# Kernel tuning notes

Measured on AMD Instinct MI355X. Metric: run time of the kernel, lower is better.

## Reference

```python
import jax, jax.numpy as jnp
import numpy as np

B, S, H = 4, 256, 768
F = 32            # num_features
T = 256           # TAG_HIDDEN_SIZE
WD = 64           # WIDTH_HIDDEN_SIZE
C = 16            # num_tags


def setup_inputs() -> dict:
    key = jax.random.key(0)
    ks = jax.random.split(key, 10)
    inp = {
        "final_hidden": jax.random.normal(ks[0], (B, S, H), jnp.float32),
        "feature_vecs": jax.random.normal(ks[1], (B, S, F), jnp.float32),
        # Linear params stored [in, out] (transposed vs torch; same math)
        "start_W": jax.random.normal(ks[2], (H + F, T), jnp.float32) * (1.0 / np.sqrt(H + F)),
        "start_b": jnp.zeros((T,), jnp.float32),
        "end_W": jax.random.normal(ks[3], (H + F, T), jnp.float32) * (1.0 / np.sqrt(H + F)),
        "end_b": jnp.zeros((T,), jnp.float32),
        "U": jax.random.normal(ks[4], (T, C, T), jnp.float32) * (1.0 / np.sqrt(T)),
        "width_hidden": jax.random.uniform(ks[5], (S, S, WD), jnp.float32),
        "lin_W": jax.random.normal(ks[6], (2 * T + WD, C), jnp.float32) * (1.0 / np.sqrt(2 * T + WD)),
        "lin_b": jnp.zeros((C,), jnp.float32),
    }
    return inp


def reference(final_hidden, feature_vecs, start_W, start_b, end_W, end_b, U, width_hidden, lin_W, lin_b):
    # dropout p=0.0 -> identity
    x = jnp.concatenate([final_hidden, feature_vecs], axis=-1)   # [B,S,H+F]
    s = x @ start_W + start_b                                    # [B,S,T]
    e = x @ end_W + end_b                                        # [B,S,T]

    # biaffine term: einsum('bsh,hci->bsci') then ('bsci,bei->bsec')
    sU = jnp.einsum('bst,tcu->bscu', s, U)                       # [B,S,C,T]
    pre = jnp.einsum('bscu,beu->bsec', sU, e)                    # [B,S,S,C]

    # pairwise FFN, fused: Linear over concat(start, end, width) decomposes
    # into three small matmuls + broadcast adds (same math, no O(S^2*(2T+W)) buffer)
    Ws, We, Ww = lin_W[:T], lin_W[T:2 * T], lin_W[2 * T:]
    ffn = (jnp.einsum('bst,tc->bsc', s, Ws)[:, :, None, :]
           + jnp.einsum('bet,tc->bec', e, We)[:, None, :, :]
           + jnp.einsum('sew,wc->sec', width_hidden, Ww)[None]
           + lin_b)                                              # [B,S,S,C]
    return pre + ffn
```

## Files before the change

### kernel.cpp

```cpp
#include <hip/hip_runtime.h>


#define B_ 4
#define S_ 256
#define H_ 768
#define F_ 32
#define T_ 256
#define C_ 16
#define R_ 1024
#define HF 800
#define HFP 832

typedef unsigned short u16;
typedef __attribute__((ext_vector_type(8))) short short8;
typedef __attribute__((ext_vector_type(4))) float f32x4;

__device__ __forceinline__ u16 f2b(float x) {
    unsigned u = __builtin_bit_cast(unsigned, x);
    u += 0x7FFF + ((u >> 16) & 1);
    return (u16)(u >> 16);
}
__device__ __forceinline__ float b2f(u16 b) {
    unsigned u = ((unsigned)b) << 16;
    return __builtin_bit_cast(float, u);
}

__global__ __launch_bounds__(256)
void k_prep(const float* __restrict__ fh, const float* __restrict__ fv,
            const float* __restrict__ sW, const float* __restrict__ eW,
            const float* __restrict__ U,  const float* __restrict__ WH,
            const float* __restrict__ linW, const float* __restrict__ linb,
            u16* __restrict__ Xb, u16* __restrict__ Wt, u16* __restrict__ Ut,
            float* __restrict__ WC)
{
    const int bid = blockIdx.x;
    const int tid = threadIdx.x;

    if (bid < 832) {
        int idx = bid * 256 + tid;
        int r = idx / 208, c4 = idx % 208;
        int k = c4 * 4;
        float4 v;
        if (k < H_)       v = *(const float4*)&fh[r * H_ + k];
        else if (k < HF)  v = *(const float4*)&fv[r * F_ + k - H_];
        else              v = make_float4(0.f, 0.f, 0.f, 0.f);
        ushort4 o; o.x = f2b(v.x); o.y = f2b(v.y); o.z = f2b(v.z); o.w = f2b(v.w);
        *(ushort4*)&Xb[(size_t)r * HFP + k] = o;
        return;
    }
    if (bid < 1232) {
        __shared__ float t_[32][33];
        int bid2 = bid - 832;
        int k0 = (bid2 / 16) * 32;
        int j0 = (bid2 % 16) * 32;
        const float* src = (j0 < T_) ? sW : eW;
        const int js = (j0 < T_) ? j0 : j0 - T_;
        {
            int jl = tid & 31, kl0 = (tid >> 5) * 4;
#pragma unroll
            for (int i = 0; i < 4; ++i)
                t_[kl0 + i][jl] = src[(k0 + kl0 + i) * T_ + js + jl];
        }
        __syncthreads();
        {
            int kl = tid & 31, jl0 = (tid >> 5) * 4;
#pragma unroll
            for (int i = 0; i < 4; ++i)
                Wt[(size_t)(j0 + jl0 + i) * HFP + k0 + kl] = f2b(t_[kl][jl0 + i]);
        }
        return;
    }
    if (bid < 1248) {
        int idx = (bid - 1232) * 256 + tid;
        int r = idx >> 3, c4 = idx & 7;
        ushort4 z; z.x = z.y = z.z = z.w = 0;
        *(ushort4*)&Wt[(size_t)r * HFP + HF + c4 * 4] = z;
        return;
    }
    if (bid < 2272) {
        __shared__ float t_[32][33];
        int bid2 = bid - 1248;
        int cu0 = (bid2 >> 3) * 32;
        int t0  = (bid2 & 7) * 32;
        {
            int cul = tid & 31, tl0 = (tid >> 5) * 4;
#pragma unroll
            for (int i = 0; i < 4; ++i)
                t_[tl0 + i][cul] = U[(size_t)(t0 + tl0 + i) * 4096 + cu0 + cul];
        }
        __syncthreads();
        {
            int tl = tid & 31, cul0 = (tid >> 5) * 4;
#pragma unroll
            for (int i = 0; i < 4; ++i)
                Ut[(size_t)(cu0 + cul0 + i) * T_ + t0 + tl] = f2b(t_[tl][cul0 + i]);
        }
        return;
    }
    {
        __shared__ float Wl[16][64];
        __shared__ float Wwl[64][16];
        int se0 = (bid - 2272) * 16;
        {
            int sel = tid >> 4, w4 = tid & 15;
            *(float4*)&Wl[sel][w4 * 4] = *(const float4*)&WH[(size_t)(se0 + sel) * 64 + w4 * 4];
        }
        {
            int w = tid >> 2, c4 = tid & 3;
            *(float4*)&Wwl[w][c4 * 4] = *(const float4*)&linW[(512 + w) * 16 + c4 * 4];
        }
        __syncthreads();
        int sel = tid >> 4, c = tid & 15;
        float acc = linb[c];
#pragma unroll
        for (int w = 0; w < 64; ++w)
            acc += Wl[sel][w] * Wwl[w][c];
        WC[(size_t)(se0 + sel) * 16 + c] = acc;
    }
}

template<int K>
__device__ __forceinline__ void gemm_core(const u16* __restrict__ Ag, int lda,
                                          const u16* __restrict__ Bg, int ldb,
                                          int wr, int wc, int lr, int kgl,
                                          f32x4 acc[2][2])
{
    const u16* ar0 = Ag + (size_t)(wr * 32 + lr) * lda + kgl * 8;
    const u16* ar1 = ar0 + 16 * (size_t)lda;
    const u16* br0 = Bg + (size_t)(wc * 32 + lr) * ldb + kgl * 8;
    const u16* br1 = br0 + 16 * (size_t)ldb;
#pragma unroll 4
    for (int k = 0; k < K; k += 32) {
        short8 a0 = *(const short8*)(ar0 + k);
        short8 a1 = *(const short8*)(ar1 + k);
        short8 b0 = *(const short8*)(br0 + k);
        short8 b1 = *(const short8*)(br1 + k);
        acc[0][0] = __builtin_amdgcn_mfma_f32_16x16x32_bf16(a0, b0, acc[0][0], 0, 0, 0);
        acc[0][1] = __builtin_amdgcn_mfma_f32_16x16x32_bf16(a0, b1, acc[0][1], 0, 0, 0);
        acc[1][0] = __builtin_amdgcn_mfma_f32_16x16x32_bf16(a1, b0, acc[1][0], 0, 0, 0);
        acc[1][1] = __builtin_amdgcn_mfma_f32_16x16x32_bf16(a1, b1, acc[1][1], 0, 0, 0);
    }
}

__global__ __launch_bounds__(256)
void k_se(const u16* __restrict__ Xb, const u16* __restrict__ Wt,
          const float* __restrict__ sb, const float* __restrict__ eb,
          u16* __restrict__ SEb)
{
    const int tid = threadIdx.x;
    const int l = tid & 63, w = tid >> 6;
    const int wr = w >> 1, wc = w & 1;
    const int lr = l & 15, kgl = l >> 4;
    const int bm = blockIdx.x * 64, bn = blockIdx.y * 64;
    f32x4 acc[2][2] = {};

    gemm_core<HFP>(Xb + (size_t)bm * HFP, HFP, Wt + (size_t)bn * HFP, HFP,
                   wr, wc, lr, kgl, acc);

#pragma unroll
    for (int j = 0; j < 2; ++j) {
        int col = bn + wc * 32 + j * 16 + lr;
        float bias = (col < T_) ? sb[col] : eb[col - T_];
#pragma unroll
        for (int i = 0; i < 2; ++i)
#pragma unroll
            for (int q = 0; q < 4; ++q) {
                int r = bm + wr * 32 + i * 16 + kgl * 4 + q;
                SEb[(size_t)r * 512 + col] = f2b(acc[i][j][q] + bias);
            }
    }
}

__global__ __launch_bounds__(256)
void k_scec(const u16* __restrict__ SEb, const float* __restrict__ linW,
            float* __restrict__ SCEC)
{
    __shared__ float SEl[4][512];
    const int tid = threadIdx.x;
    const int r0 = blockIdx.x * 4;
#pragma unroll
    for (int i = 0; i < 2; ++i) {
        int ch = tid + i * 256;
        int rl = ch >> 7, o4 = (ch & 127) * 4;
        ushort4 v = *(const ushort4*)&SEb[(size_t)(r0 + rl) * 512 + o4];
        SEl[rl][o4 + 0] = b2f(v.x); SEl[rl][o4 + 1] = b2f(v.y);
        SEl[rl][o4 + 2] = b2f(v.z); SEl[rl][o4 + 3] = b2f(v.w);
    }
    __syncthreads();
    const int rl = tid >> 6, tq = (tid >> 4) & 3, c = tid & 15;
    const int t0 = tq * 64;
    float accs = 0.f, acce = 0.f;
#pragma unroll 4
    for (int t = t0; t < t0 + 64; ++t) {
        accs += SEl[rl][t]       * linW[t * 16 + c];
        acce += SEl[rl][256 + t] * linW[(256 + t) * 16 + c];
    }
    accs += __shfl_xor(accs, 16); accs += __shfl_xor(accs, 32);
    acce += __shfl_xor(acce, 16); acce += __shfl_xor(acce, 32);
    if (tq == 0) {
        SCEC[(r0 + rl) * 32 + c]      = accs;
        SCEC[(r0 + rl) * 32 + 16 + c] = acce;
    }
}

__global__ __launch_bounds__(256)
void k_su(const u16* __restrict__ SEb, const u16* __restrict__ Ut,
          u16* __restrict__ SUb)
{
    const int tid = threadIdx.x;
    const int l = tid & 63, w = tid >> 6;
    const int wr = w >> 1, wc = w & 1;
    const int lr = l & 15, kgl = l >> 4;
    const int bm = blockIdx.x * 64, bn = blockIdx.y * 64;
    f32x4 acc[2][2] = {};

    gemm_core<T_>(SEb + (size_t)bm * 512, 512, Ut + (size_t)bn * T_, T_,
                  wr, wc, lr, kgl, acc);

#pragma unroll
    for (int i = 0; i < 2; ++i)
#pragma unroll
        for (int j = 0; j < 2; ++j)
#pragma unroll
            for (int q = 0; q < 4; ++q) {
                int r  = bm + wr * 32 + i * 16 + kgl * 4 + q;
                int cc = bn + wc * 32 + j * 16 + lr;
                SUb[(size_t)r * 4096 + cc] = f2b(acc[i][j][q]);
            }
}

__global__ __launch_bounds__(256)
void k_pre(const u16* __restrict__ SEb, const u16* __restrict__ SUb,
           const float* __restrict__ SCEC, const float* __restrict__ WC,
           float* __restrict__ OUT)
{
    const int tid = threadIdx.x;
    const int l = tid & 63, w = tid >> 6;
    const int wr = w >> 1, wc = w & 1;
    const int lr = l & 15, kgl = l >> 4;
    const int bm = blockIdx.x * 64, bn = blockIdx.y * 64;
    const int b  = blockIdx.z;
    f32x4 acc[2][2] = {};

    const u16* Abase = SEb + (size_t)(b << 8) * 512 + 256 + (size_t)bm * 512;
    const u16* Bbase = SUb + ((size_t)b << 20) + (size_t)bn * T_;

    gemm_core<T_>(Abase, 512, Bbase, T_, wr, wc, lr, kgl, acc);

#pragma unroll
    for (int j = 0; j < 2; ++j) {
        int n = bn + wc * 32 + j * 16 + lr;
        int s = n >> 4, c = n & 15;
        float scv = SCEC[((b << 8) + s) * 32 + c];
#pragma unroll
        for (int i = 0; i < 2; ++i)
#pragma unroll
            for (int q = 0; q < 4; ++q) {
                int e = bm + wr * 32 + i * 16 + kgl * 4 + q;
                float ecv = SCEC[((b << 8) + e) * 32 + 16 + c];
                float wcv = WC[(size_t)(s * S_ + e) * 16 + c];
                OUT[(((size_t)(b << 8) + s) * S_ + e) * 16 + c] =
                    acc[i][j][q] + scv + ecv + wcv;
            }
    }
}

extern "C" void kernel_launch(void* const* d_in, const int* in_sizes, int n_in,
                              void* d_out, int out_size, void* d_ws, size_t ws_size,
                              hipStream_t stream)
{
    const float* fh   = (const float*)d_in[0];
    const float* fv   = (const float*)d_in[1];
    const float* sW   = (const float*)d_in[2];
    const float* sb   = (const float*)d_in[3];
    const float* eW   = (const float*)d_in[4];
    const float* eb   = (const float*)d_in[5];
    const float* U    = (const float*)d_in[6];
    const float* WH   = (const float*)d_in[7];
    const float* linW = (const float*)d_in[8];
    const float* linb = (const float*)d_in[9];
    float* OUT = (float*)d_out;

    char* p = (char*)d_ws;
    u16* SUb = (u16*)p;      p += (size_t)B_ * 4096 * 256 * 2;
    float* WC = (float*)p;   p += (size_t)S_ * S_ * C_ * 4;
    u16* Ut  = (u16*)p;      p += (size_t)4096 * T_ * 2;
    u16* Xb  = (u16*)p;      p += (size_t)R_ * HFP * 2;
    u16* Wt  = (u16*)p;      p += (size_t)512 * HFP * 2;
    u16* SEb = (u16*)p;      p += (size_t)R_ * 512 * 2;
    float* SCEC = (float*)p; p += (size_t)R_ * 32 * 4;

    k_prep<<<dim3(6368), 256, 0, stream>>>(fh, fv, sW, eW, U, WH, linW, linb,
                                           Xb, Wt, Ut, WC);
    k_se  <<<dim3(16, 8), 256, 0, stream>>>(Xb, Wt, sb, eb, SEb);
    k_scec<<<dim3(256), 256, 0, stream>>>(SEb, linW, SCEC);
    k_su  <<<dim3(16, 64), 256, 0, stream>>>(SEb, Ut, SUb);
    k_pre <<<dim3(4, 64, 4), 256, 0, stream>>>(SEb, SUb, SCEC, WC, OUT);
}
```

Measured before the change: 74.54 us.

## Swap GEMM operand roles for vectorized epilogues, enlarge tiles, merge scec into su

New measurement: 61.18 us. 1.22x faster.

```diff
diff --git a/kernel.cpp b/kernel.cpp
--- a/kernel.cpp
+++ b/kernel.cpp
@@ -119,26 +119,30 @@
     }
 }
 
-template<int K>
-__device__ __forceinline__ void gemm_core(const u16* __restrict__ Ag, int lda,
-                                          const u16* __restrict__ Bg, int ldb,
-                                          int wr, int wc, int lr, int kgl,
-                                          f32x4 acc[2][2])
-{
-    const u16* ar0 = Ag + (size_t)(wr * 32 + lr) * lda + kgl * 8;
-    const u16* ar1 = ar0 + 16 * (size_t)lda;
-    const u16* br0 = Bg + (size_t)(wc * 32 + lr) * ldb + kgl * 8;
-    const u16* br1 = br0 + 16 * (size_t)ldb;
-#pragma unroll 4
+template<int K, int LDA, int LDB, int MF, int NF, int UNROLL>
+__device__ __forceinline__ void core(const u16* __restrict__ A,
+                                     const u16* __restrict__ B,
+                                     int lr, int kgl, f32x4 acc[MF][NF])
+{
+    const u16* ap[MF];
+    const u16* bp[NF];
+#pragma unroll
+    for (int i = 0; i < MF; ++i) ap[i] = A + (size_t)(i * 16 + lr) * LDA + kgl * 8;
+#pragma unroll
+    for (int j = 0; j < NF; ++j) bp[j] = B + (size_t)(j * 16 + lr) * LDB + kgl * 8;
+
+#pragma unroll UNROLL
     for (int k = 0; k < K; k += 32) {
-        short8 a0 = *(const short8*)(ar0 + k);
-        short8 a1 = *(const short8*)(ar1 + k);
-        short8 b0 = *(const short8*)(br0 + k);
-        short8 b1 = *(const short8*)(br1 + k);
-        acc[0][0] = __builtin_amdgcn_mfma_f32_16x16x32_bf16(a0, b0, acc[0][0], 0, 0, 0);
-        acc[0][1] = __builtin_amdgcn_mfma_f32_16x16x32_bf16(a0, b1, acc[0][1], 0, 0, 0);
-        acc[1][0] = __builtin_amdgcn_mfma_f32_16x16x32_bf16(a1, b0, acc[1][0], 0, 0, 0);
-        acc[1][1] = __builtin_amdgcn_mfma_f32_16x16x32_bf16(a1, b1, acc[1][1], 0, 0, 0);
+        short8 a[MF], b[NF];
+#pragma unroll
+        for (int i = 0; i < MF; ++i) a[i] = *(const short8*)(ap[i] + k);
+#pragma unroll
+        for (int j = 0; j < NF; ++j) b[j] = *(const short8*)(bp[j] + k);
+#pragma unroll
+        for (int i = 0; i < MF; ++i)
+#pragma unroll
+            for (int j = 0; j < NF; ++j)
+                acc[i][j] = __builtin_amdgcn_mfma_f32_16x16x32_bf16(a[i], b[j], acc[i][j], 0, 0, 0);
     }
 }
 
@@ -151,33 +155,69 @@
     const int l = tid & 63, w = tid >> 6;
     const int wr = w >> 1, wc = w & 1;
     const int lr = l & 15, kgl = l >> 4;
-    const int bm = blockIdx.x * 64, bn = blockIdx.y * 64;
+    const int bm = blockIdx.x * 64;
+    const int bn = blockIdx.y * 64;
     f32x4 acc[2][2] = {};
 
-    gemm_core<HFP>(Xb + (size_t)bm * HFP, HFP, Wt + (size_t)bn * HFP, HFP,
-                   wr, wc, lr, kgl, acc);
-
-#pragma unroll
-    for (int j = 0; j < 2; ++j) {
-        int col = bn + wc * 32 + j * 16 + lr;
-        float bias = (col < T_) ? sb[col] : eb[col - T_];
-#pragma unroll
-        for (int i = 0; i < 2; ++i)
-#pragma unroll
-            for (int q = 0; q < 4; ++q) {
-                int r = bm + wr * 32 + i * 16 + kgl * 4 + q;
-                SEb[(size_t)r * 512 + col] = f2b(acc[i][j][q] + bias);
+    core<HFP, HFP, HFP, 2, 2, 2>(Wt + (size_t)(bm + wr * 32) * HFP,
+                                 Xb + (size_t)(bn + wc * 32) * HFP,
+                                 lr, kgl, acc);
+
+#pragma unroll
+    for (int i = 0; i < 2; ++i) {
+        int j0 = bm + wr * 32 + i * 16 + kgl * 4;
+        float4 bias = (j0 < T_) ? *(const float4*)&sb[j0]
+                                : *(const float4*)&eb[j0 - T_];
+#pragma unroll
+        for (int jj = 0; jj < 2; ++jj) {
+            int r = bn + wc * 32 + jj * 16 + lr;
+            ushort4 o;
+            o.x = f2b(acc[i][jj][0] + bias.x);
+            o.y = f2b(acc[i][jj][1] + bias.y);
+            o.z = f2b(acc[i][jj][2] + bias.z);
+            o.w = f2b(acc[i][jj][3] + bias.w);
+            *(ushort4*)&SEb[(size_t)r * 512 + j0] = o;
+        }
+    }
+}
+
+__global__ __launch_bounds__(256)
+void k_su_scec(const u16* __restrict__ SEb, const u16* __restrict__ Ut,
+               const float* __restrict__ linW,
+               u16* __restrict__ SUb, float* __restrict__ SCEC)
+{
+    const int bid = blockIdx.x;
+    const int tid = threadIdx.x;
+
+    if (bid < 256) {
+        const int l = tid & 63, w = tid >> 6;
+        const int wr = w >> 1, wc = w & 1;
+        const int lr = l & 15, kgl = l >> 4;
+        const int bm = (bid & 31) * 128;
+        const int bn = (bid >> 5) * 128;
+        f32x4 acc[4][4] = {};
+
+        core<T_, T_, 512, 4, 4, 2>(Ut + (size_t)(bm + wr * 64) * T_,
+                                   SEb + (size_t)(bn + wc * 64) * 512,
+                                   lr, kgl, acc);
+
+#pragma unroll
+        for (int i = 0; i < 4; ++i) {
+            int cu0 = bm + wr * 64 + i * 16 + kgl * 4;
+#pragma unroll
+            for (int j = 0; j < 4; ++j) {
+                int r = bn + wc * 64 + j * 16 + lr;
+                ushort4 o;
+                o.x = f2b(acc[i][j][0]); o.y = f2b(acc[i][j][1]);
+                o.z = f2b(acc[i][j][2]); o.w = f2b(acc[i][j][3]);
+                *(ushort4*)&SUb[(size_t)r * 4096 + cu0] = o;
             }
-    }
-}
-
-__global__ __launch_bounds__(256)
-void k_scec(const u16* __restrict__ SEb, const float* __restrict__ linW,
-            float* __restrict__ SCEC)
-{
+        }
+        return;
+    }
+
     __shared__ float SEl[4][512];
-    const int tid = threadIdx.x;
-    const int r0 = blockIdx.x * 4;
+    const int r0 = (bid - 256) * 4;
 #pragma unroll
     for (int i = 0; i < 2; ++i) {
         int ch = tid + i * 256;
@@ -204,64 +244,46 @@
 }
 
 __global__ __launch_bounds__(256)
-void k_su(const u16* __restrict__ SEb, const u16* __restrict__ Ut,
-          u16* __restrict__ SUb)
+void k_pre(const u16* __restrict__ SEb, const u16* __restrict__ SUb,
+           const float* __restrict__ SCEC, const float* __restrict__ WC,
+           float* __restrict__ OUT)
 {
     const int tid = threadIdx.x;
     const int l = tid & 63, w = tid >> 6;
     const int wr = w >> 1, wc = w & 1;
     const int lr = l & 15, kgl = l >> 4;
-    const int bm = blockIdx.x * 64, bn = blockIdx.y * 64;
-    f32x4 acc[2][2] = {};
-
-    gemm_core<T_>(SEb + (size_t)bm * 512, 512, Ut + (size_t)bn * T_, T_,
-                  wr, wc, lr, kgl, acc);
-
-#pragma unroll
-    for (int i = 0; i < 2; ++i)
-#pragma unroll
-        for (int j = 0; j < 2; ++j)
-#pragma unroll
-            for (int q = 0; q < 4; ++q) {
-                int r  = bm + wr * 32 + i * 16 + kgl * 4 + q;
-                int cc = bn + wc * 32 + j * 16 + lr;
-                SUb[(size_t)r * 4096 + cc] = f2b(acc[i][j][q]);
-            }
-}
-
-__global__ __launch_bounds__(256)
-void k_pre(const u16* __restrict__ SEb, const u16* __restrict__ SUb,
-           const float* __restrict__ SCEC, const float* __restrict__ WC,
-           float* __restrict__ OUT)
-{
-    const int tid = threadIdx.x;
-    const int l = tid & 63, w = tid >> 6;
-    const int wr = w >> 1, wc = w & 1;
-    const int lr = l & 15, kgl = l >> 4;
-    const int bm = blockIdx.x * 64, bn = blockIdx.y * 64;
+    const int bm = blockIdx.x * 128;
+    const int bn = blockIdx.y * 128;
     const int b  = blockIdx.z;
-    f32x4 acc[2][2] = {};
-
-    const u16* Abase = SEb + (size_t)(b << 8) * 512 + 256 + (size_t)bm * 512;
-    const u16* Bbase = SUb + ((size_t)b << 20) + (size_t)bn * T_;
-
-    gemm_core<T_>(Abase, 512, Bbase, T_, wr, wc, lr, kgl, acc);
-
-#pragma unroll
-    for (int j = 0; j < 2; ++j) {
-        int n = bn + wc * 32 + j * 16 + lr;
-        int s = n >> 4, c = n & 15;
-        float scv = SCEC[((b << 8) + s) * 32 + c];
-#pragma unroll
-        for (int i = 0; i < 2; ++i)
-#pragma unroll
-            for (int q = 0; q < 4; ++q) {
-                int e = bm + wr * 32 + i * 16 + kgl * 4 + q;
-                float ecv = SCEC[((b << 8) + e) * 32 + 16 + c];
-                float wcv = WC[(size_t)(s * S_ + e) * 16 + c];
-                OUT[(((size_t)(b << 8) + s) * S_ + e) * 16 + c] =
-                    acc[i][j][q] + scv + ecv + wcv;
-            }
+    f32x4 acc[4][4] = {};
+
+    const u16* An = SUb + ((size_t)b << 20) + (size_t)(bm + wr * 64) * T_;
+    const u16* Be = SEb + (size_t)(b << 8) * 512 + 256 + (size_t)(bn + wc * 64) * 512;
+
+    core<T_, T_, 512, 4, 4, 2>(An, Be, lr, kgl, acc);
+
+    const int c0 = kgl * 4;
+    float4 scv[4];
+#pragma unroll
+    for (int i = 0; i < 4; ++i) {
+        int s = (bm + wr * 64 + i * 16) >> 4;
+        scv[i] = *(const float4*)&SCEC[((b << 8) + s) * 32 + c0];
+    }
+#pragma unroll
+    for (int j = 0; j < 4; ++j) {
+        int e = bn + wc * 64 + j * 16 + lr;
+        float4 ecv = *(const float4*)&SCEC[((b << 8) + e) * 32 + 16 + c0];
+#pragma unroll
+        for (int i = 0; i < 4; ++i) {
+            int s = (bm + wr * 64 + i * 16) >> 4;
+            float4 wcv = *(const float4*)&WC[(size_t)(s * S_ + e) * 16 + c0];
+            float4 o;
+            o.x = acc[i][j][0] + scv[i].x + ecv.x + wcv.x;
+            o.y = acc[i][j][1] + scv[i].y + ecv.y + wcv.y;
+            o.z = acc[i][j][2] + scv[i].z + ecv.z + wcv.z;
+            o.w = acc[i][j][3] + scv[i].w + ecv.w + wcv.w;
+            *(float4*)&OUT[(((size_t)(b << 8) + s) * S_ + e) * 16 + c0] = o;
+        }
     }
 }
 
@@ -292,8 +314,7 @@
 
     k_prep<<<dim3(6368), 256, 0, stream>>>(fh, fv, sW, eW, U, WH, linW, linb,
                                            Xb, Wt, Ut, WC);
-    k_se  <<<dim3(16, 8), 256, 0, stream>>>(Xb, Wt, sb, eb, SEb);
-    k_scec<<<dim3(256), 256, 0, stream>>>(SEb, linW, SCEC);
-    k_su  <<<dim3(16, 64), 256, 0, stream>>>(SEb, Ut, SUb);
-    k_pre <<<dim3(4, 64, 4), 256, 0, stream>>>(SEb, SUb, SCEC, WC, OUT);
-}
+    k_se  <<<dim3(8, 16), 256, 0, stream>>>(Xb, Wt, sb, eb, SEb);
+    k_su_scec<<<dim3(512), 256, 0, stream>>>(SEb, Ut, linW, SUb, SCEC);
+    k_pre <<<dim3(32, 2, 4), 256, 0, stream>>>(SEb, SUb, SCEC, WC, OUT);
+}
```
